# Optimization experiments

Measured on AMD Instinct MI355X. Metric: run time of the kernel, lower is better.

Reference implementation:

```python
import jax, jax.numpy as jnp
import numpy as np

N_NODES = 50000
N_EDGES = 800000
F_IN = 32
H = 128
LN_EPS = 1e-5


def _gcn_layer(h, src, tgt, w_self, b_self, w_neigh, b_neigh):
    # h: [N, D]; src/tgt: [E]
    n = h.shape[0]
    self_feat = h @ w_self + b_self                      # [N, Dout]
    src_feat = h[src]                                    # [E, D] gather
    agg = jax.ops.segment_sum(src_feat, tgt, num_segments=n)          # [N, D]
    cnt = jax.ops.segment_sum(jnp.ones((src.shape[0],), h.dtype), tgt,
                              num_segments=n)[:, None]   # [N, 1]
    agg = agg / jnp.maximum(cnt, 1.0)
    return self_feat + agg @ w_neigh + b_neigh


def _layer_norm(x, gamma, beta):
    mu = jnp.mean(x, axis=-1, keepdims=True)
    var = jnp.mean(jnp.square(x - mu), axis=-1, keepdims=True)
    return (x - mu) * jax.lax.rsqrt(var + LN_EPS) * gamma + beta


def setup_inputs() -> dict:
    key = jax.random.key(0)
    ks = jax.random.split(key, 16)
    s_in = 1.0 / np.sqrt(F_IN)
    s_h = 1.0 / np.sqrt(H)
    inp = {
        "x": jax.random.normal(ks[0], (N_NODES, F_IN), jnp.float32),
        "edge_index": jax.random.randint(ks[1], (2, N_EDGES), 0, N_NODES, jnp.int64)
        if jax.config.jax_enable_x64 else
        jax.random.randint(ks[1], (2, N_EDGES), 0, N_NODES, jnp.int32),
        "w_in": jax.random.uniform(ks[2], (F_IN, H), jnp.float32, -s_in, s_in),
        "b_in": jax.random.uniform(ks[3], (H,), jnp.float32, -s_in, s_in),
        "ws0": jax.random.uniform(ks[4], (H, H), jnp.float32, -s_h, s_h),
        "bs0": jax.random.uniform(ks[5], (H,), jnp.float32, -s_h, s_h),
        "wn0": jax.random.uniform(ks[6], (H, H), jnp.float32, -s_h, s_h),
        "bn0": jax.random.uniform(ks[7], (H,), jnp.float32, -s_h, s_h),
        "g0": jnp.ones((H,), jnp.float32),
        "be0": jnp.zeros((H,), jnp.float32),
        "ws1": jax.random.uniform(ks[8], (H, H), jnp.float32, -s_h, s_h),
        "bs1": jax.random.uniform(ks[9], (H,), jnp.float32, -s_h, s_h),
        "wn1": jax.random.uniform(ks[10], (H, H), jnp.float32, -s_h, s_h),
        "bn1": jax.random.uniform(ks[11], (H,), jnp.float32, -s_h, s_h),
        "g1": jnp.ones((H,), jnp.float32),
        "be1": jnp.zeros((H,), jnp.float32),
    }
    return inp


def reference(x, edge_index, w_in, b_in, ws0, bs0, wn0, bn0, g0, be0,
              ws1, bs1, wn1, bn1, g1, be1):
    src, tgt = edge_index[0], edge_index[1]
    h = jax.nn.relu(x @ w_in + b_in)                     # input_proj + relu
    # layer 0 (intermediate): gcn -> LN -> relu -> dropout(eval=id) -> residual
    residual = h
    h = _gcn_layer(h, src, tgt, ws0, bs0, wn0, bn0)
    h = _layer_norm(h, g0, be0)
    h = jax.nn.relu(h) + residual
    # layer 1 (final): gcn -> LN
    h = _gcn_layer(h, src, tgt, ws1, bs1, wn1, bn1)
    h = _layer_norm(h, g1, be1)
    return h
```

## Files before the change

### kernel.cpp

```cpp
#include <hip/hip_runtime.h>

#define H 128
#define CAP 64
typedef unsigned short ushort_t;
typedef __bf16 bf16x8 __attribute__((ext_vector_type(8)));
typedef unsigned short u16x8 __attribute__((ext_vector_type(8)));
typedef float f32x4 __attribute__((ext_vector_type(4)));
typedef float f32x2 __attribute__((ext_vector_type(2)));

__device__ __forceinline__ float bf2f(ushort_t b) {
    return __uint_as_float(((unsigned int)b) << 16);
}
__device__ __forceinline__ ushort_t f2bf(float f) {
    unsigned int u = __float_as_uint(f);
    unsigned int r = (u + 0x7fffu + ((u >> 16) & 1u)) >> 16;
    return (ushort_t)r;
}
__device__ __forceinline__ unsigned char f2fp8(float f) {
    int r = __builtin_amdgcn_cvt_pk_fp8_f32(f, f, 0, false);
    return (unsigned char)(r & 0xff);
}
__device__ __forceinline__ void acc8(float* s, uint2 v) {
    f32x2 a0 = __builtin_amdgcn_cvt_pk_f32_fp8(v.x, false);
    f32x2 a1 = __builtin_amdgcn_cvt_pk_f32_fp8(v.x, true);
    f32x2 a2 = __builtin_amdgcn_cvt_pk_f32_fp8(v.y, false);
    f32x2 a3 = __builtin_amdgcn_cvt_pk_f32_fp8(v.y, true);
    s[0] += a0.x; s[1] += a0.y; s[2] += a1.x; s[3] += a1.y;
    s[4] += a2.x; s[5] += a2.y; s[6] += a3.x; s[7] += a3.y;
}

__device__ __forceinline__
void pack_one(int idx, const float* __restrict__ W0, const float* __restrict__ W1,
              const float* __restrict__ b0, const float* __restrict__ b1,
              ushort_t* __restrict__ Wpack, float* __restrict__ bsum,
              int Ksplit, int K)
{
    int total = K * 16;
    if (idx < total) {
        int l = idx & 63, tt = (idx >> 6) & 7, s = idx >> 9;
        int c = tt * 16 + (l & 15);
        int kb = s * 32 + ((l >> 4) & 3) * 8;
#pragma unroll
        for (int j = 0; j < 8; ++j) {
            int k = kb + j;
            float v = (k < Ksplit) ? W0[(size_t)k * H + c]
                                   : W1[(size_t)(k - Ksplit) * H + c];
            Wpack[(size_t)idx * 8 + j] = f2bf(v);
        }
    }
    if (idx < H) bsum[idx] = b0[idx] + (b1 ? b1[idx] : 0.f);
}

__global__ __launch_bounds__(256)
void k_prep(const float* __restrict__ w_in, const float* __restrict__ b_in,
            const float* __restrict__ ws0, const float* __restrict__ bs0,
            const float* __restrict__ wn0, const float* __restrict__ bn0,
            const float* __restrict__ ws1, const float* __restrict__ bs1,
            const float* __restrict__ wn1, const float* __restrict__ bn1,
            ushort_t* __restrict__ Wpin, float* __restrict__ bin,
            ushort_t* __restrict__ Wp0, float* __restrict__ bsm0,
            ushort_t* __restrict__ Wp1, float* __restrict__ bsm1,
            int* __restrict__ fl, int N)
{
    int b = blockIdx.x, t = threadIdx.x;
    if (b < 2) {
        pack_one(b * 256 + t, w_in, w_in, b_in, nullptr, Wpin, bin, 32, 32);
    } else if (b < 18) {
        pack_one((b - 2) * 256 + t, ws0, wn0, bs0, bn0, Wp0, bsm0, 128, 256);
    } else if (b < 34) {
        pack_one((b - 18) * 256 + t, ws1, wn1, bs1, bn1, Wp1, bsm1, 128, 256);
    } else {
        int i = (b - 34) * 256 + t;
        if (i < N) fl[i] = 0;
    }
}

#define FILL_CHUNK 4096

__device__ __forceinline__
void fill_body(int blk, const int* __restrict__ srcs, const int* __restrict__ tgts,
               int* __restrict__ fl, ushort_t* __restrict__ col, int E)
{
    int range = blk & 7;
    int chunk = blk >> 3;
    int base = chunk * FILL_CHUNK;
    int t = threadIdx.x;
    int i0 = base + t * 4;
    int4 tg[4], sr[4];
#pragma unroll
    for (int u = 0; u < 4; ++u) {
        int idx = i0 + u * 1024;
        if (idx + 3 < E) {
            tg[u] = *(const int4*)(tgts + idx);
            sr[u] = *(const int4*)(srcs + idx);
        } else {
            int v[4] = {-1, -1, -1, -1}, s[4] = {0, 0, 0, 0};
#pragma unroll
            for (int j = 0; j < 4; ++j)
                if (idx + j < E) { v[j] = tgts[idx + j]; s[j] = srcs[idx + j]; }
            tg[u] = make_int4(v[0], v[1], v[2], v[3]);
            sr[u] = make_int4(s[0], s[1], s[2], s[3]);
        }
    }
#pragma unroll
    for (int u = 0; u < 4; ++u) {
        int tv[4] = {tg[u].x, tg[u].y, tg[u].z, tg[u].w};
        int sv[4] = {sr[u].x, sr[u].y, sr[u].z, sr[u].w};
#pragma unroll
        for (int j = 0; j < 4; ++j) {
            int tt = tv[j];
            if (tt >= 0 && (tt >> 13) == range) {
                int p = atomicAdd(&fl[tt], 1);
                if (p < CAP) col[tt * CAP + p] = (ushort_t)sv[j];
            }
        }
    }
}

template<int K, int DO_LN, int RESREL, int RELU, int OUTBF, int HQ, int AF32>
__device__ __forceinline__
void gemm_body(int bidm,
               const ushort_t* __restrict__ A, const float* __restrict__ Af, int lda,
               const ushort_t* __restrict__ Wpack,
               const float* __restrict__ bias,
               const float* __restrict__ g, const float* __restrict__ be,
               const ushort_t* __restrict__ resid, int ldr,
               float* __restrict__ Cf, ushort_t* __restrict__ Cb,
               unsigned char* __restrict__ hq, int ldc, int M)
{
    constexpr int NS = K / 32;
    __shared__ ushort_t Bs[NS * 8 * 64 * 8];
    const int t = threadIdx.x;
    {
        const uint4* wsrc = (const uint4*)Wpack;
        uint4* wdst = (uint4*)Bs;
        constexpr int CH = K * 16;
#pragma unroll
        for (int i = t; i < CH; i += 256) wdst[i] = wsrc[i];
    }
    __syncthreads();

    const int wave = t >> 6, lane = t & 63;
    const int quad = lane >> 4, l16 = lane & 15;
    const int m0 = bidm * 128 + wave * 32;

    f32x4 acc[2][8];
#pragma unroll
    for (int mt = 0; mt < 2; ++mt)
#pragma unroll
        for (int nt = 0; nt < 8; ++nt) acc[mt][nt] = (f32x4){0.f, 0.f, 0.f, 0.f};

    bf16x8 afrag[NS][2];
#pragma unroll
    for (int s = 0; s < NS; ++s)
#pragma unroll
        for (int mt = 0; mt < 2; ++mt) {
            int row = m0 + mt * 16 + l16;
            if (row >= M) row = M - 1;
            if (AF32) {
                const float* p = Af + (size_t)row * lda + s * 32 + quad * 8;
                float4 v0 = *(const float4*)p;
                float4 v1 = *(const float4*)(p + 4);
                union { u16x8 u; bf16x8 b; } cv;
                cv.u[0] = f2bf(v0.x); cv.u[1] = f2bf(v0.y);
                cv.u[2] = f2bf(v0.z); cv.u[3] = f2bf(v0.w);
                cv.u[4] = f2bf(v1.x); cv.u[5] = f2bf(v1.y);
                cv.u[6] = f2bf(v1.z); cv.u[7] = f2bf(v1.w);
                afrag[s][mt] = cv.b;
            } else {
                afrag[s][mt] = *(const bf16x8*)(A + (size_t)row * lda + s * 32 + quad * 8);
            }
        }

    const bf16x8* bfr = (const bf16x8*)Bs;
#pragma unroll
    for (int s = 0; s < NS; ++s)
#pragma unroll
        for (int nt = 0; nt < 8; ++nt) {
            bf16x8 b = bfr[(s * 8 + nt) * 64 + lane];
#pragma unroll
            for (int mt = 0; mt < 2; ++mt)
                acc[mt][nt] = __builtin_amdgcn_mfma_f32_16x16x32_bf16(
                    afrag[s][mt], b, acc[mt][nt], 0, 0, 0);
        }

    float bv[8], gv[8], bev[8];
#pragma unroll
    for (int nt = 0; nt < 8; ++nt) {
        int c = nt * 16 + l16;
        bv[nt] = bias[c];
        if (DO_LN) { gv[nt] = g[c]; bev[nt] = be[c]; }
    }

#pragma unroll
    for (int mt = 0; mt < 2; ++mt)
#pragma unroll
        for (int r = 0; r < 4; ++r) {
            int row = m0 + mt * 16 + quad * 4 + r;
            float v[8];
#pragma unroll
            for (int nt = 0; nt < 8; ++nt) v[nt] = acc[mt][nt][r] + bv[nt];
            if (DO_LN) {
                float s1 = 0.f, s2 = 0.f;
#pragma unroll
                for (int nt = 0; nt < 8; ++nt) { s1 += v[nt]; s2 += v[nt] * v[nt]; }
#pragma unroll
                for (int mk = 1; mk < 16; mk <<= 1) {
                    s1 += __shfl_xor(s1, mk);
                    s2 += __shfl_xor(s2, mk);
                }
                float mu = s1 * (1.f / H);
                float var = s2 * (1.f / H) - mu * mu;
                float rs = rsqrtf(var + 1e-5f);
#pragma unroll
                for (int nt = 0; nt < 8; ++nt)
                    v[nt] = (v[nt] - mu) * rs * gv[nt] + bev[nt];
            }
            if (row < M) {
#pragma unroll
                for (int nt = 0; nt < 8; ++nt) {
                    int c = nt * 16 + l16;
                    float y = v[nt];
                    if (RELU) y = fmaxf(y, 0.f);
                    if (RESREL)
                        y = fmaxf(y, 0.f) + bf2f(resid[(size_t)row * ldr + c]);
                    if (OUTBF) Cb[(size_t)row * ldc + c] = f2bf(y);
                    else       Cf[(size_t)row * ldc + c] = y;
                    if (HQ) hq[(size_t)row * H + c] = f2fp8(y);
                }
            }
        }
}

__global__ __launch_bounds__(256)
void k_gin(const float* __restrict__ x, const ushort_t* __restrict__ Wpin,
           const float* __restrict__ bin,
           ushort_t* __restrict__ Cb, unsigned char* __restrict__ hq,
           const int* __restrict__ srcs, const int* __restrict__ tgts,
           int* __restrict__ fl, ushort_t* __restrict__ col, int E,
           int fillBlocks, int M)
{
    if ((int)blockIdx.x < fillBlocks) {
        fill_body(blockIdx.x, srcs, tgts, fl, col, E);
        return;
    }
    gemm_body<32, 0, 0, 1, 1, 1, 1>(blockIdx.x - fillBlocks,
        nullptr, x, 32, Wpin, bin, nullptr, nullptr, nullptr, 0,
        nullptr, Cb, hq, 256, M);
}

__global__ __launch_bounds__(256)
void k_gl0(const ushort_t* __restrict__ A, const ushort_t* __restrict__ Wp,
           const float* __restrict__ bias,
           const float* __restrict__ g, const float* __restrict__ be,
           ushort_t* __restrict__ Cb, unsigned char* __restrict__ hq, int M)
{
    gemm_body<256, 1, 1, 0, 1, 1, 0>(blockIdx.x,
        A, nullptr, 256, Wp, bias, g, be, A, 256,
        nullptr, Cb, hq, 256, M);
}

__global__ __launch_bounds__(256)
void k_gl1(const ushort_t* __restrict__ A, const ushort_t* __restrict__ Wp,
           const float* __restrict__ bias,
           const float* __restrict__ g, const float* __restrict__ be,
           float* __restrict__ Cf, int M)
{
    gemm_body<256, 1, 0, 0, 0, 0, 0>(blockIdx.x,
        A, nullptr, 256, Wp, bias, g, be, nullptr, 0,
        Cf, nullptr, nullptr, H, M);
}

__device__ __forceinline__
void agg_body(const unsigned char* __restrict__ hq, const int* __restrict__ fl,
              const ushort_t* __restrict__ col, ushort_t* __restrict__ out, int n)
{
    int node = blockIdx.x * 4 + (threadIdx.x >> 6);
    if (node >= n) return;
    int lane = threadIdx.x & 63;
    int grp = lane >> 4, li = lane & 15;
    int cnt = fl[node];
    int m = cnt < CAP ? cnt : CAP;
    int beg = node * CAP, end = beg + m;
    float s[8];
#pragma unroll
    for (int j = 0; j < 8; ++j) s[j] = 0.f;

    int e = beg;
    for (; e + 16 <= end; e += 16) {
        uint2 v[4];
#pragma unroll
        for (int q = 0; q < 4; ++q) {
            int r = col[e + 4 * q + grp];
            v[q] = *(const uint2*)(hq + (size_t)r * 128 + li * 8);
        }
#pragma unroll
        for (int q = 0; q < 4; ++q) acc8(s, v[q]);
    }
    if (e + 8 <= end) {
        uint2 v[2];
#pragma unroll
        for (int q = 0; q < 2; ++q) {
            int r = col[e + 4 * q + grp];
            v[q] = *(const uint2*)(hq + (size_t)r * 128 + li * 8);
        }
#pragma unroll
        for (int q = 0; q < 2; ++q) acc8(s, v[q]);
        e += 8;
    }
    if (e + 4 <= end) {
        int r = col[e + grp];
        uint2 v0 = *(const uint2*)(hq + (size_t)r * 128 + li * 8);
        acc8(s, v0);
        e += 4;
    }
    for (; e < end; ++e) {
        if (grp == 0) {
            int r = col[e];
            uint2 v0 = *(const uint2*)(hq + (size_t)r * 128 + li * 8);
            acc8(s, v0);
        }
    }
#pragma unroll
    for (int j = 0; j < 8; ++j) {
        s[j] += __shfl_xor(s[j], 16);
        s[j] += __shfl_xor(s[j], 32);
    }
    if (grp == 0) {
        float inv = 1.f / fmaxf((float)cnt, 1.f);
        uint4 o;
        o.x = ((unsigned)f2bf(s[1] * inv) << 16) | f2bf(s[0] * inv);
        o.y = ((unsigned)f2bf(s[3] * inv) << 16) | f2bf(s[2] * inv);
        o.z = ((unsigned)f2bf(s[5] * inv) << 16) | f2bf(s[4] * inv);
        o.w = ((unsigned)f2bf(s[7] * inv) << 16) | f2bf(s[6] * inv);
        *(uint4*)(out + (size_t)node * 256 + li * 8) = o;
    }
}

__global__ __launch_bounds__(256)
void k_agg0(const unsigned char* __restrict__ hq, const int* __restrict__ fl,
            const ushort_t* __restrict__ col, ushort_t* __restrict__ out, int n)
{ agg_body(hq, fl, col, out, n); }

__global__ __launch_bounds__(256)
void k_agg1(const unsigned char* __restrict__ hq, const int* __restrict__ fl,
            const ushort_t* __restrict__ col, ushort_t* __restrict__ out, int n)
{ agg_body(hq, fl, col, out, n); }

extern "C" void kernel_launch(void* const* d_in, const int* in_sizes, int n_in,
                              void* d_out, int out_size, void* d_ws, size_t ws_size,
                              hipStream_t stream)
{
    const float* x    = (const float*)d_in[0];
    const int*   ei   = (const int*)d_in[1];
    const float* w_in = (const float*)d_in[2];
    const float* b_in = (const float*)d_in[3];
    const float* ws0  = (const float*)d_in[4];
    const float* bs0  = (const float*)d_in[5];
    const float* wn0  = (const float*)d_in[6];
    const float* bn0  = (const float*)d_in[7];
    const float* g0   = (const float*)d_in[8];
    const float* be0  = (const float*)d_in[9];
    const float* ws1  = (const float*)d_in[10];
    const float* bs1  = (const float*)d_in[11];
    const float* wn1  = (const float*)d_in[12];
    const float* bn1  = (const float*)d_in[13];
    const float* g1   = (const float*)d_in[14];
    const float* be1  = (const float*)d_in[15];

    const int N = in_sizes[0] / 32;
    const int E = in_sizes[1] / 2;
    const int* srcs = ei;
    const int* tgts = ei + E;

    char* w = (char*)d_ws;
    ushort_t* Acat0 = (ushort_t*)w;  w += (size_t)N * 256 * 2;
    ushort_t* Acat1 = (ushort_t*)w;  w += (size_t)N * 256 * 2;
    unsigned char* hq0 = (unsigned char*)w;  w += (size_t)N * H;
    unsigned char* hq1 = (unsigned char*)w;  w += (size_t)N * H;
    ushort_t* Wpin  = (ushort_t*)w;  w += 32 * H * 2;
    ushort_t* Wp0   = (ushort_t*)w;  w += 256 * H * 2;
    ushort_t* Wp1   = (ushort_t*)w;  w += 256 * H * 2;
    float* bin  = (float*)w;         w += H * 4;
    float* bsm0 = (float*)w;         w += H * 4;
    float* bsm1 = (float*)w;         w += H * 4;
    int* fl     = (int*)w;           w += (size_t)N * 4;
    ushort_t* col = (ushort_t*)w;    w += (size_t)N * CAP * 2;

    int gN = (N + 255) / 256;
    int gM = (N + 127) / 128;
    int gF = 8 * ((E + FILL_CHUNK - 1) / FILL_CHUNK);

    k_prep<<<34 + gN, 256, 0, stream>>>(
        w_in, b_in, ws0, bs0, wn0, bn0, ws1, bs1, wn1, bn1,
        Wpin, bin, Wp0, bsm0, Wp1, bsm1, fl, N);

    k_gin<<<gF + gM, 256, 0, stream>>>(
        x, Wpin, bin, Acat0, hq0, srcs, tgts, fl, col, E, gF, N);

    k_agg0<<<(N + 3) / 4, 256, 0, stream>>>(hq0, fl, col, Acat0 + 128, N);
    k_gl0<<<gM, 256, 0, stream>>>(Acat0, Wp0, bsm0, g0, be0, Acat1, hq1, N);

    k_agg1<<<(N + 3) / 4, 256, 0, stream>>>(hq1, fl, col, Acat1 + 128, N);
    k_gl1<<<gM, 256, 0, stream>>>(Acat1, Wp1, bsm1, g1, be1, (float*)d_out, N);
}
```

Before: 229.2 us.

## Process two nodes per wave in aggregation and simplify edge fill loop

The aggregation kernel now has each wave handle two destination nodes. It interleaves their gathered fp8 row loads in 16-edge steps with masked tails, which raises memory-level parallelism and halves the grid size. The edge fill loop is replaced by a simple strided scalar loop in place of the unrolled int4 vector loads. The trade-offs are masked wasted lanes when the two nodes' degrees differ, and less vectorised loading in the fill stage.

```diff
diff --git a/kernel.cpp b/kernel.cpp
--- a/kernel.cpp
+++ b/kernel.cpp
@@ -83,36 +83,13 @@
 {
     int range = blk & 7;
     int chunk = blk >> 3;
-    int base = chunk * FILL_CHUNK;
-    int t = threadIdx.x;
-    int i0 = base + t * 4;
-    int4 tg[4], sr[4];
-#pragma unroll
-    for (int u = 0; u < 4; ++u) {
-        int idx = i0 + u * 1024;
-        if (idx + 3 < E) {
-            tg[u] = *(const int4*)(tgts + idx);
-            sr[u] = *(const int4*)(srcs + idx);
-        } else {
-            int v[4] = {-1, -1, -1, -1}, s[4] = {0, 0, 0, 0};
-#pragma unroll
-            for (int j = 0; j < 4; ++j)
-                if (idx + j < E) { v[j] = tgts[idx + j]; s[j] = srcs[idx + j]; }
-            tg[u] = make_int4(v[0], v[1], v[2], v[3]);
-            sr[u] = make_int4(s[0], s[1], s[2], s[3]);
-        }
-    }
-#pragma unroll
-    for (int u = 0; u < 4; ++u) {
-        int tv[4] = {tg[u].x, tg[u].y, tg[u].z, tg[u].w};
-        int sv[4] = {sr[u].x, sr[u].y, sr[u].z, sr[u].w};
-#pragma unroll
-        for (int j = 0; j < 4; ++j) {
-            int tt = tv[j];
-            if (tt >= 0 && (tt >> 13) == range) {
-                int p = atomicAdd(&fl[tt], 1);
-                if (p < CAP) col[tt * CAP + p] = (ushort_t)sv[j];
-            }
+    int lim = chunk * FILL_CHUNK + FILL_CHUNK;
+    if (lim > E) lim = E;
+    for (int i = chunk * FILL_CHUNK + threadIdx.x; i < lim; i += 256) {
+        int tt = tgts[i];
+        if ((tt >> 13) == range) {
+            int p = atomicAdd(&fl[tt], 1);
+            if (p < CAP) col[tt * CAP + p] = (ushort_t)srcs[i];
         }
     }
 }
@@ -272,80 +249,76 @@
 }
 
 __device__ __forceinline__
-void agg_body(const unsigned char* __restrict__ hq, const int* __restrict__ fl,
+void agg_body(int blk, const unsigned char* __restrict__ hq,
+              const int* __restrict__ fl,
               const ushort_t* __restrict__ col, ushort_t* __restrict__ out, int n)
 {
-    int node = blockIdx.x * 4 + (threadIdx.x >> 6);
-    if (node >= n) return;
+    int wave = threadIdx.x >> 6;
     int lane = threadIdx.x & 63;
     int grp = lane >> 4, li = lane & 15;
-    int cnt = fl[node];
-    int m = cnt < CAP ? cnt : CAP;
-    int beg = node * CAP, end = beg + m;
-    float s[8];
-#pragma unroll
-    for (int j = 0; j < 8; ++j) s[j] = 0.f;
-
-    int e = beg;
-    for (; e + 16 <= end; e += 16) {
-        uint2 v[4];
-#pragma unroll
-        for (int q = 0; q < 4; ++q) {
-            int r = col[e + 4 * q + grp];
-            v[q] = *(const uint2*)(hq + (size_t)r * 128 + li * 8);
-        }
-#pragma unroll
-        for (int q = 0; q < 4; ++q) acc8(s, v[q]);
-    }
-    if (e + 8 <= end) {
-        uint2 v[2];
-#pragma unroll
-        for (int q = 0; q < 2; ++q) {
-            int r = col[e + 4 * q + grp];
-            v[q] = *(const uint2*)(hq + (size_t)r * 128 + li * 8);
-        }
-#pragma unroll
-        for (int q = 0; q < 2; ++q) acc8(s, v[q]);
-        e += 8;
-    }
-    if (e + 4 <= end) {
-        int r = col[e + grp];
-        uint2 v0 = *(const uint2*)(hq + (size_t)r * 128 + li * 8);
-        acc8(s, v0);
-        e += 4;
-    }
-    for (; e < end; ++e) {
-        if (grp == 0) {
-            int r = col[e];
-            uint2 v0 = *(const uint2*)(hq + (size_t)r * 128 + li * 8);
-            acc8(s, v0);
-        }
-    }
-#pragma unroll
-    for (int j = 0; j < 8; ++j) {
-        s[j] += __shfl_xor(s[j], 16);
-        s[j] += __shfl_xor(s[j], 32);
-    }
-    if (grp == 0) {
-        float inv = 1.f / fmaxf((float)cnt, 1.f);
+    int n0 = blk * 8 + wave * 2;
+    if (n0 >= n) return;
+
+    int cnt[2], m[2];
+#pragma unroll
+    for (int u = 0; u < 2; ++u) {
+        int nd = n0 + u;
+        cnt[u] = (nd < n) ? fl[nd] : 0;
+        m[u] = cnt[u] < CAP ? cnt[u] : CAP;
+    }
+    float s[2][8];
+#pragma unroll
+    for (int u = 0; u < 2; ++u)
+#pragma unroll
+        for (int j = 0; j < 8; ++j) s[u][j] = 0.f;
+
+    int mx = m[0] > m[1] ? m[0] : m[1];
+    for (int e = 0; e < mx; e += 16) {
+        uint2 v[2][4];
+#pragma unroll
+        for (int u = 0; u < 2; ++u)
+#pragma unroll
+            for (int q = 0; q < 4; ++q) {
+                int idx = e + q * 4 + grp;
+                bool val = idx < m[u];
+                int r = val ? (int)col[(n0 + u) * CAP + idx] : 0;
+                uint2 tv = {0u, 0u};
+                if (val) tv = *(const uint2*)(hq + (size_t)r * 128 + li * 8);
+                v[u][q] = tv;
+            }
+#pragma unroll
+        for (int u = 0; u < 2; ++u)
+#pragma unroll
+            for (int q = 0; q < 4; ++q) acc8(s[u], v[u][q]);
+    }
+#pragma unroll
+    for (int u = 0; u < 2; ++u)
+#pragma unroll
+        for (int j = 0; j < 8; ++j) {
+            s[u][j] += __shfl_xor(s[u][j], 16);
+            s[u][j] += __shfl_xor(s[u][j], 32);
+        }
+    if (grp < 2 && (n0 + grp) < n) {
+        int u = grp;
+        float inv = 1.f / fmaxf((float)cnt[u], 1.f);
         uint4 o;
-        o.x = ((unsigned)f2bf(s[1] * inv) << 16) | f2bf(s[0] * inv);
-        o.y = ((unsigned)f2bf(s[3] * inv) << 16) | f2bf(s[2] * inv);
-        o.z = ((unsigned)f2bf(s[5] * inv) << 16) | f2bf(s[4] * inv);
-        o.w = ((unsigned)f2bf(s[7] * inv) << 16) | f2bf(s[6] * inv);
-        *(uint4*)(out + (size_t)node * 256 + li * 8) = o;
+        o.x = ((unsigned)f2bf(s[u][1] * inv) << 16) | f2bf(s[u][0] * inv);
+        o.y = ((unsigned)f2bf(s[u][3] * inv) << 16) | f2bf(s[u][2] * inv);
+        o.z = ((unsigned)f2bf(s[u][5] * inv) << 16) | f2bf(s[u][4] * inv);
+        o.w = ((unsigned)f2bf(s[u][7] * inv) << 16) | f2bf(s[u][6] * inv);
+        *(uint4*)(out + (size_t)(n0 + u) * 256 + li * 8) = o;
     }
 }
 
 __global__ __launch_bounds__(256)
 void k_agg0(const unsigned char* __restrict__ hq, const int* __restrict__ fl,
             const ushort_t* __restrict__ col, ushort_t* __restrict__ out, int n)
-{ agg_body(hq, fl, col, out, n); }
+{ agg_body(blockIdx.x, hq, fl, col, out, n); }
 
 __global__ __launch_bounds__(256)
 void k_agg1(const unsigned char* __restrict__ hq, const int* __restrict__ fl,
             const ushort_t* __restrict__ col, ushort_t* __restrict__ out, int n)
-{ agg_body(hq, fl, col, out, n); }
+{ agg_body(blockIdx.x, hq, fl, col, out, n); }
 
 extern "C" void kernel_launch(void* const* d_in, const int* in_sizes, int n_in,
                               void* d_out, int out_size, void* d_ws, size_t ws_size,
@@ -389,6 +362,7 @@
 
     int gN = (N + 255) / 256;
     int gM = (N + 127) / 128;
+    int gA = (N + 7) / 8;
     int gF = 8 * ((E + FILL_CHUNK - 1) / FILL_CHUNK);
 
     k_prep<<<34 + gN, 256, 0, stream>>>(
@@ -398,9 +372,9 @@
     k_gin<<<gF + gM, 256, 0, stream>>>(
         x, Wpin, bin, Acat0, hq0, srcs, tgts, fl, col, E, gF, N);
 
-    k_agg0<<<(N + 3) / 4, 256, 0, stream>>>(hq0, fl, col, Acat0 + 128, N);
+    k_agg0<<<gA, 256, 0, stream>>>(hq0, fl, col, Acat0 + 128, N);
     k_gl0<<<gM, 256, 0, stream>>>(Acat0, Wp0, bsm0, g0, be0, Acat1, hq1, N);
 
-    k_agg1<<<(N + 3) / 4, 256, 0, stream>>>(hq1, fl, col, Acat1 + 128, N);
+    k_agg1<<<gA, 256, 0, stream>>>(hq1, fl, col, Acat1 + 128, N);
     k_gl1<<<gM, 256, 0, stream>>>(Acat1, Wp1, bsm1, g1, be1, (float*)d_out, N);
 }
```

After: 233.9 us. 1.02x slower.
